# Kernel tuning notes

Hardware: AMD Instinct MI355X
Metric: run time of the kernel (lower is better)

Reference implementation:

```python
import jax, jax.numpy as jnp
from jax import lax
import numpy as np

B, C, H, W, OUTC, KS = 4, 64, 128, 128, 64, 3
N = KS * KS
PAD = 1
STRIDE = 1


def conv2d(x, w, b, stride, pad):
    out = lax.conv_general_dilated(x, w, (stride, stride), ((pad, pad), (pad, pad)),
                                   dimension_numbers=('NCHW', 'OIHW', 'NCHW'))
    if b is not None:
        out = out + b[None, :, None, None]
    return out


def setup_inputs() -> dict:
    key = jax.random.key(0)
    k = jax.random.split(key, 8)
    f = jnp.float32

    def w_init(kk, shape, fan_in, scale=1.0):
        return jax.random.normal(kk, shape, f) * (scale / np.sqrt(fan_in))

    return {
        'x': jax.random.normal(k[0], (B, C, H, W), f),
        'ref': jax.random.normal(k[1], (B, C, H, W), f),
        'w_cd': w_init(k[2], (C, 2 * C, 1, 1), 2 * C),
        'b_cd': jnp.zeros((C,), f),
        'w_p': w_init(k[3], (2 * N, C, 3, 3), C * 9, 0.1),  # small offsets, keeps sampling stable
        'b_p': jnp.zeros((2 * N,), f),
        'w_m': w_init(k[4], (N, C, 3, 3), C * 9),
        'b_m': jnp.zeros((N,), f),
        'w_c': w_init(k[5], (N * C, C, 3, 3), C * 9),
        'b_c': jnp.zeros((N * C,), f),
        'w_conv': w_init(k[6], (OUTC, C, KS, KS), C * KS * KS),
    }


def deform_forward(x, ref, w_cd, b_cd, w_p, b_p, w_m, b_m, w_c, b_c, w_conv):
    b, c, h, w = x.shape
    fused = conv2d(jnp.concatenate([x, ref], axis=1), w_cd, b_cd, 1, 0)
    offset = conv2d(fused, w_p, b_p, STRIDE, 1)             # [b, 2N, h, w]
    m = jax.nn.sigmoid(conv2d(fused, w_m, b_m, STRIDE, 1))  # [b, N, h, w]
    c_off = jnp.tanh(conv2d(fused, w_c, b_c, STRIDE, 1))    # [b, N*c, h, w]

    xp = jnp.pad(x, ((0, 0), (0, 0), (PAD, PAD), (PAD, PAD)))
    Hp, Wp = h + 2 * PAD, w + 2 * PAD

    # kernel-relative grid p_n (first N entries = rows, last N = cols)
    r = jnp.arange(-(KS - 1) // 2, (KS - 1) // 2 + 1)
    pnx, pny = jnp.meshgrid(r, r, indexing='ij')
    p_n = jnp.concatenate([pnx.ravel(), pny.ravel()]).reshape(1, 2 * N, 1, 1)
    # base grid p_0 starts at 1 because of the zero padding
    gx, gy = jnp.meshgrid(jnp.arange(1, h * STRIDE + 1, STRIDE),
                          jnp.arange(1, w * STRIDE + 1, STRIDE), indexing='ij')
    p_0 = jnp.concatenate([jnp.broadcast_to(gx[None, None], (1, N, h, w)),
                           jnp.broadcast_to(gy[None, None], (1, N, h, w))], axis=1)
    p = (p_0 + p_n).astype(offset.dtype) + offset           # [b, 2N, h, w]
    p = p.transpose(0, 2, 3, 1)                             # [b, h, w, 2N]

    q_lt = jnp.floor(lax.stop_gradient(p))
    q_rb = q_lt + 1

    def clampq(q):
        return jnp.concatenate([jnp.clip(q[..., :N], 0, Hp - 1),
                                jnp.clip(q[..., N:], 0, Wp - 1)], axis=-1).astype(jnp.int32)

    q_lt = clampq(q_lt)
    q_rb = clampq(q_rb)
    q_lb = jnp.concatenate([q_lt[..., :N], q_rb[..., N:]], axis=-1)
    q_rt = jnp.concatenate([q_rb[..., :N], q_lt[..., N:]], axis=-1)
    p = jnp.concatenate([jnp.clip(p[..., :N], 0, Hp - 1),
                         jnp.clip(p[..., N:], 0, Wp - 1)], axis=-1)

    def gweight(q, sx, sy):
        qx = q[..., :N].astype(p.dtype)
        qy = q[..., N:].astype(p.dtype)
        return (1 + sx * (qx - p[..., :N])) * (1 + sy * (qy - p[..., N:]))

    g_lt = gweight(q_lt, 1, 1)
    g_rb = gweight(q_rb, -1, -1)
    g_lb = gweight(q_lb, 1, -1)
    g_rt = gweight(q_rt, -1, 1)

    x_flat = xp.reshape(b, c, Hp * Wp)

    def get_x_q(q):
        idx = q[..., :N] * Wp + q[..., N:]                  # [b, h, w, N]
        xq = jnp.take_along_axis(x_flat, idx.reshape(b, 1, -1), axis=2)
        return xq.reshape(b, c, h, w, N)

    x_off = (g_lt[:, None] * get_x_q(q_lt) + g_rb[:, None] * get_x_q(q_rb)
             + g_lb[:, None] * get_x_q(q_lb) + g_rt[:, None] * get_x_q(q_rt))

    # color deformation: [b, N*c, h, w] -> [b, c, h, w, N]
    x_off = x_off + c_off.reshape(b, c, N, h, w).transpose(0, 1, 3, 4, 2)
    # modulation broadcast over channels
    x_off = x_off * m.transpose(0, 2, 3, 1)[:, None]

    # [b,c,h,w,N] -> [b,c,h*ks,w*ks] with N = (kernel_row, kernel_col)
    x_off = x_off.reshape(b, c, h, w, KS, KS).transpose(0, 1, 2, 4, 3, 5)
    x_off = x_off.reshape(b, c, h * KS, w * KS)
    return conv2d(x_off, w_conv, None, KS, 0)


def reference(x, ref, w_cd, b_cd, w_p, b_p, w_m, b_m, w_c, b_c, w_conv):
    return deform_forward(x, ref, w_cd, b_cd, w_p, b_p, w_m, b_m, w_c, b_c, w_conv)
```

## Files before the change

### kernel.cpp

```cpp
#include <hip/hip_runtime.h>
#include <hip/hip_fp16.h>


typedef __attribute__((ext_vector_type(8))) __bf16 bf16x8;
typedef __attribute__((ext_vector_type(16))) float f32x16;
#define MFMA32(a, b, c) __builtin_amdgcn_mfma_f32_32x32x16_bf16((a), (b), (c), 0, 0, 0)

#define WS_AC    0
#define WS_APM   368640
#define WS_ACONV 387072
#define WS_F2    436224

struct f2pair { float x, y; };

__device__ __forceinline__ unsigned short f2bf(float f) {
    unsigned u = __float_as_uint(f);
    return (unsigned short)((u + 0x7FFFu + ((u >> 16) & 1u)) >> 16);
}
__device__ __forceinline__ float fast_rcp(float x) {
#if __has_builtin(__builtin_amdgcn_rcpf)
    return __builtin_amdgcn_rcpf(x);
#else
    return 1.0f / x;
#endif
}
__device__ __forceinline__ float fast_tanh(float x) {
    float t = __expf(2.0f * x);
    return 1.0f - 2.0f * fast_rcp(t + 1.0f);
}
__device__ __forceinline__ float fast_sigmoid(float x) {
    return fast_rcp(1.0f + __expf(-x));
}

__device__ __forceinline__ uint4 stage_load64(const unsigned short* f2b, int h,
                                              int px0, int chunk, int tid) {
    int tap = chunk >> 1;
    int dh = tap / 3 - 1, dw = tap % 3 - 1;
    int hs = h + dh;
    int kg = tid >> 6, px = tid & 63;
    int cg = (chunk & 1) * 4 + kg;
    int wsrc = px0 + px + dw;
    uint4 pk = {0u, 0u, 0u, 0u};
    if (((unsigned)hs < 128u) && ((unsigned)wsrc < 128u))
        pk = *(const uint4*)(f2b + (((size_t)cg << 14) + (hs << 7) + wsrc) * 8);
    return pk;
}
__device__ __forceinline__ void stage_write64(char* Bst, uint4 pk, int tid) {
    int kg = tid >> 6, px = tid & 63;
    *(uint4*)(Bst + ((kg >> 1) * 2 + (px >> 5)) * 1024
                  + ((px & 31) + 32 * (kg & 1)) * 16) = pk;
}

__global__ __launch_bounds__(256, 4)
void k2_fused(const float* __restrict__ x, const float* __restrict__ ref,
              const float* __restrict__ b_cd, const float* __restrict__ w_c,
              const float* __restrict__ w_p, const float* __restrict__ w_m,
              const float* __restrict__ w_conv, const float* __restrict__ w_cd,
              unsigned short* __restrict__ ws) {
    __shared__ __align__(16) char B0[32768];
    __shared__ __align__(16) unsigned short WcdL[8192];
    const int tid = threadIdx.x, l = tid & 63, w = tid >> 6;
    const int b = blockIdx.y, p0 = blockIdx.x * 128;
    const int rl31 = l & 31, kh8 = (l >> 5) * 8;

    {
        int gtid = (blockIdx.y * 128 + blockIdx.x) * 256 + tid;
        #pragma unroll 1
        for (int i = gtid; i < 428032; i += 131072) {
            float val;
            if (i < WS_APM) {
                int t = i, jj = t & 7, lx = (t >> 3) & 63, r = t >> 9;
                int ks = r % 36, gmt = r / 36;
                int row = gmt * 32 + (lx & 31);
                int kp = ks * 16 + (lx >> 5) * 8 + jj, tap = kp >> 6, ci = kp & 63;
                val = (row < 576) ? w_c[row * 576 + ci * 9 + tap] : 0.0f;
            } else if (i < WS_ACONV) {
                int t = i - WS_APM, jj = t & 7, lx = (t >> 3) & 63, ks = t >> 9;
                int row = lx & 31;
                int kp = ks * 16 + (lx >> 5) * 8 + jj, tap = kp >> 6, ci = kp & 63;
                val = (row < 18) ? w_p[row * 576 + ci * 9 + tap]
                    : (row < 27) ? w_m[(row - 18) * 576 + ci * 9 + tap] : 0.0f;
            } else {
                int t = i - WS_ACONV, jj = t & 7, lx = (t >> 3) & 63, r = t >> 9;
                int gks = r % 40, ocT2 = r / 40;
                int oc = ocT2 * 32 + (lx & 31);
                int krow = gks * 16 + (lx >> 5) * 8 + jj;
                val = (krow < 576) ? w_conv[oc * 576 + krow] : 0.0f;
            }
            ws[i] = f2bf(val);
        }
    }
    #pragma unroll
    for (int i = tid; i < 8192; i += 256) WcdL[i] = f2bf(w_cd[i]);

    #pragma unroll
    for (int it = 0; it < 8; ++it) {
        int task = it * 256 + tid;
        int kg = task >> 7, px = task & 127;
        const float* src = (kg < 8) ? x : ref;
        int kbase = (kg & 7) * 8;
        unsigned short v[8];
        #pragma unroll
        for (int j = 0; j < 8; ++j)
            v[j] = f2bf(src[(((size_t)b * 64 + kbase + j) << 14) + p0 + px]);
        uint4 pk;
        pk.x = (unsigned)v[0] | ((unsigned)v[1] << 16);
        pk.y = (unsigned)v[2] | ((unsigned)v[3] << 16);
        pk.z = (unsigned)v[4] | ((unsigned)v[5] << 16);
        pk.w = (unsigned)v[6] | ((unsigned)v[7] << 16);
        *(uint4*)(B0 + ((kg >> 1) * 4 + (px >> 5)) * 1024
                      + ((px & 31) + 32 * (kg & 1)) * 16) = pk;
    }
    __syncthreads();

    f32x16 a0, a1;
    #pragma unroll
    for (int r = 0; r < 16; ++r) { a0[r] = 0.0f; a1[r] = 0.0f; }
    const unsigned short* A0 = WcdL + rl31 * 128 + kh8;
    #pragma unroll
    for (int s = 0; s < 8; ++s) {
        bf16x8 bf = *(bf16x8*)(B0 + ((s * 4 + w) * 64 + l) * 16);
        bf16x8 x0 = *(const bf16x8*)(A0 + s * 16);
        bf16x8 x1 = *(const bf16x8*)(A0 + 32 * 128 + s * 16);
        a0 = MFMA32(x0, bf, a0);
        a1 = MFMA32(x1, bf, a1);
    }
    unsigned short* f2 = ws + WS_F2 + ((size_t)b << 20);
    int px = p0 + w * 32 + rl31;
    int h4 = (l >> 5) * 4;
    #pragma unroll
    for (int t = 0; t < 2; ++t)
        #pragma unroll
        for (int q = 0; q < 4; ++q) {
            ushort4 st;
            float v0 = (t ? a1[q * 4 + 0] : a0[q * 4 + 0]) + b_cd[t * 32 + 8 * q + h4 + 0];
            float v1 = (t ? a1[q * 4 + 1] : a0[q * 4 + 1]) + b_cd[t * 32 + 8 * q + h4 + 1];
            float v2 = (t ? a1[q * 4 + 2] : a0[q * 4 + 2]) + b_cd[t * 32 + 8 * q + h4 + 2];
            float v3 = (t ? a1[q * 4 + 3] : a0[q * 4 + 3]) + b_cd[t * 32 + 8 * q + h4 + 3];
            st.x = f2bf(v0); st.y = f2bf(v1); st.z = f2bf(v2); st.w = f2bf(v3);
            *(ushort4*)(f2 + ((size_t)((t * 4 + q) << 14) + px) * 8 + h4) = st;
        }
}

__global__ __launch_bounds__(256, 4)
void k3_main(const float* __restrict__ x, const float* __restrict__ b_c,
             const float* __restrict__ b_p, const float* __restrict__ b_m,
             const unsigned short* __restrict__ wsbf, float* __restrict__ out) {
    __shared__ __align__(16) char lds[36096];
    char* Bst0 = lds;
    char* Bst1 = lds + 4096;
    char* Amod = lds + 8192;
    float* uL = (float*)(lds + 8192);
    char* tbl = lds + 24576;
    float* bcL = (float*)(lds + 33792);

    const int tid = threadIdx.x, l = tid & 63, w = tid >> 6;
    const int lh = l >> 5, l31 = l & 31;
    const int id = blockIdx.x;
    const int hbLin = (id & 7) * 128 + (id >> 3);
    const int half = hbLin & 1, b = (hbLin >> 1) & 3, h = hbLin >> 3;
    const int px0 = half * 64;
    const unsigned short* f2b = wsbf + WS_F2 + ((size_t)b << 20);
    const float* xb = x + (((size_t)b * 64) << 14);
    const int ocT = w >> 1, nT2 = w & 1;

    for (int i = tid; i < 576; i += 256) bcL[i] = b_c[i];

    f32x16 oa;

    auto epi = [&](f32x16& a, int j, int rowbase) {
        const int pxe = j * 32 + l31;
        if (rowbase < 576) {
            #pragma unroll
            for (int reg = 0; reg < 16; ++reg) {
                int rl = (reg & 3) + 8 * (reg >> 2) + 4 * lh;
                int row = rowbase + rl;
                int c = row / 9, n = row - c * 9;
                float uv = a[reg] + bcL[row];
                float t = fast_tanh(uv);
                uint4 rec = *(const uint4*)(tbl + (pxe * 9 + n) * 16);
                float w0 = __half2float(__ushort_as_half((unsigned short)(rec.x & 0xffffu)));
                float w1 = __half2float(__ushort_as_half((unsigned short)(rec.x >> 16)));
                float w2 = __half2float(__ushort_as_half((unsigned short)(rec.y & 0xffffu)));
                float w3 = __half2float(__ushort_as_half((unsigned short)(rec.y >> 16)));
                int i0 = (int)(rec.z & 0xffffu);
                int i1 = (int)(rec.z >> 16);
                float mval = __uint_as_float(rec.w);
                const float* xp = xb + ((size_t)c << 14);
                f2pair v0 = *(const f2pair*)(xp + i0);
                f2pair v1 = *(const f2pair*)(xp + i1);
                float samp = w0 * v0.x + w1 * v0.y + w2 * v1.x + w3 * v1.y;
                a[reg] = mval * (samp + t);
                if ((reg & 3) == 3) __builtin_amdgcn_sched_barrier(0);
            }
        } else {
            #pragma unroll
            for (int reg = 0; reg < 16; ++reg) a[reg] = 0.0f;
        }
    };
    auto scat = [&](const f32x16& a, int j) {
        #pragma unroll
        for (int reg = 0; reg < 16; ++reg) {
            int rl = (reg & 3) + 8 * (reg >> 2) + 4 * lh;
            int k = w * 32 + rl;
            *(unsigned short*)(Amod + ((k >> 4) * 2 + j) * 1024
                    + (l31 + 32 * ((k >> 3) & 1)) * 16 + (k & 7) * 2)
                = f2bf(a[reg]);
        }
    };

    {
        f32x16 acc0, acc1, pm;
        #pragma unroll
        for (int r = 0; r < 16; ++r) { acc0[r] = 0.0f; acc1[r] = 0.0f; pm[r] = 0.0f; }
        stage_write64(Bst0, stage_load64(f2b, h, px0, 0, tid), tid);
        __syncthreads();
        #pragma unroll 1
        for (int it = 0; it < 18; ++it) {
            char* cur = (it & 1) ? Bst1 : Bst0;
            char* nxt = (it & 1) ? Bst0 : Bst1;
            uint4 pk;
            if (it < 17) pk = stage_load64(f2b, h, px0, it + 1, tid);
            #pragma unroll
            for (int s = 0; s < 2; ++s) {
                const int ks = it * 2 + s;
                bf16x8 bf0 = *(bf16x8*)(cur + ((s * 2 + 0) * 64 + l) * 16);
                bf16x8 bf1 = *(bf16x8*)(cur + ((s * 2 + 1) * 64 + l) * 16);
                bf16x8 af = *(const bf16x8*)(wsbf + WS_AC
                                + (((w * 36 + ks) * 64 + l) << 3));
                acc0 = MFMA32(af, bf0, acc0);
                acc1 = MFMA32(af, bf1, acc1);
                if (w < 2) {
                    bf16x8 apm = *(const bf16x8*)(wsbf + WS_APM + ((ks * 64 + l) << 3));
                    pm = MFMA32(apm, w ? bf1 : bf0, pm);
                }
            }
            if (it < 17) stage_write64(nxt, pk, tid);
            __syncthreads();
        }
        if (w < 2) {
            int pxp = w * 32 + l31;
            #pragma unroll
            for (int reg = 0; reg < 16; ++reg) {
                int rl = (reg & 3) + 8 * (reg >> 2) + 4 * lh;
                uL[rl * 64 + pxp] = pm[reg];
            }
        }
        __syncthreads();

        #pragma unroll 1
        for (int i = tid; i < 576; i += 256) {
            int n = i >> 6, px = i & 63;
            float offr = uL[n * 64 + px] + b_p[n];
            float offc = uL[(9 + n) * 64 + px] + b_p[9 + n];
            float mraw = uL[(18 + n) * 64 + px] + b_m[n];
            int nr = n / 3, nc = n - nr * 3;
            float pr = (float)(h + nr) + offr;
            float pc = (float)(px0 + px + nc) + offc;
            float flr = floorf(pr), flc = floorf(pc);
            float prc = fminf(fmaxf(pr, 0.0f), 129.0f);
            float pcc = fminf(fmaxf(pc, 0.0f), 129.0f);
            float q0r = fminf(fmaxf(flr, 0.0f), 129.0f);
            float q1r = fminf(fmaxf(flr + 1.0f, 0.0f), 129.0f);
            int ir0 = (int)q0r, ir1 = (int)q1r;
            bool vr0 = (ir0 >= 1) && (ir0 <= 128), vr1 = (ir1 >= 1) && (ir1 <= 128);
            float wr0 = vr0 ? (1.0f + q0r - prc) : 0.0f;
            float wr1 = vr1 ? (1.0f - (q1r - prc)) : 0.0f;
            float q0c = fminf(fmaxf(flc, 0.0f), 129.0f);
            float q1c = fminf(fmaxf(flc + 1.0f, 0.0f), 129.0f);
            int ic0 = (int)q0c, ic1 = (int)q1c;
            bool vc0 = (ic0 >= 1) && (ic0 <= 128), vc1 = (ic1 >= 1) && (ic1 <= 128);
            float wc0 = vc0 ? (1.0f + q0c - pcc) : 0.0f;
            float wc1 = vc1 ? (1.0f - (q1c - pcc)) : 0.0f;
            int cx0 = ic0 - 1, cx1 = ic1 - 1;
            int base = min(max(cx0, 0), 126);
            float ws0 = ((base == cx0) && vc0 ? wc0 : 0.0f)
                      + ((base == cx1) && vc1 ? wc1 : 0.0f);
            float ws1 = ((base + 1 == cx0) && vc0 ? wc0 : 0.0f)
                      + ((base + 1 == cx1) && vc1 ? wc1 : 0.0f);
            int rx0 = min(max(ir0 - 1, 0), 127), rx1 = min(max(ir1 - 1, 0), 127);
            uint4 rec;
            rec.x = (unsigned)__half_as_ushort(__float2half(wr0 * ws0))
                  | ((unsigned)__half_as_ushort(__float2half(wr0 * ws1)) << 16);
            rec.y = (unsigned)__half_as_ushort(__float2half(wr1 * ws0))
                  | ((unsigned)__half_as_ushort(__float2half(wr1 * ws1)) << 16);
            rec.z = (unsigned)(unsigned short)(rx0 * 128 + base)
                  | ((unsigned)(unsigned short)(rx1 * 128 + base) << 16);
            rec.w = __float_as_uint(fast_sigmoid(mraw));
            *(uint4*)(tbl + (px * 9 + n) * 16) = rec;
        }
        __syncthreads();

        epi(acc0, 0, w * 32);
        epi(acc1, 1, w * 32);
        #pragma unroll
        for (int r = 0; r < 16; ++r) oa[r] = 0.0f;
        scat(acc0, 0);
        scat(acc1, 1);
        __syncthreads();
        #pragma unroll
        for (int ks8 = 0; ks8 < 8; ++ks8) {
            bf16x8 af = *(const bf16x8*)(wsbf + WS_ACONV
                            + (((ocT * 40 + ks8) * 64 + l) << 3));
            bf16x8 bf = *(bf16x8*)(Amod + (ks8 * 2 + nT2) * 1024 + l * 16);
            oa = MFMA32(af, bf, oa);
        }
    }

    #pragma unroll 1
    for (int p = 1; p < 5; ++p) {
        const int mt = p * 4 + w;
        f32x16 acc0, acc1;
        #pragma unroll
        for (int r = 0; r < 16; ++r) { acc0[r] = 0.0f; acc1[r] = 0.0f; }

        stage_write64(Bst0, stage_load64(f2b, h, px0, 0, tid), tid);
        __syncthreads();
        #pragma unroll 1
        for (int it = 0; it < 18; ++it) {
            char* cur = (it & 1) ? Bst1 : Bst0;
            char* nxt = (it & 1) ? Bst0 : Bst1;
            uint4 pk;
            if (it < 17) pk = stage_load64(f2b, h, px0, it + 1, tid);
            #pragma unroll
            for (int s = 0; s < 2; ++s) {
                const int ks = it * 2 + s;
                bf16x8 bf0 = *(bf16x8*)(cur + ((s * 2 + 0) * 64 + l) * 16);
                bf16x8 bf1 = *(bf16x8*)(cur + ((s * 2 + 1) * 64 + l) * 16);
                bf16x8 af = *(const bf16x8*)(wsbf + WS_AC
                                + (((mt * 36 + ks) * 64 + l) << 3));
                acc0 = MFMA32(af, bf0, acc0);
                acc1 = MFMA32(af, bf1, acc1);
            }
            if (it < 17) stage_write64(nxt, pk, tid);
            __syncthreads();
        }

        epi(acc0, 0, mt * 32);
        epi(acc1, 1, mt * 32);

        __syncthreads();
        scat(acc0, 0);
        scat(acc1, 1);
        __syncthreads();
        #pragma unroll
        for (int ks8 = 0; ks8 < 8; ++ks8) {
            bf16x8 af = *(const bf16x8*)(wsbf + WS_ACONV
                            + (((ocT * 40 + p * 8 + ks8) * 64 + l) << 3));
            bf16x8 bf = *(bf16x8*)(Amod + (ks8 * 2 + nT2) * 1024 + l * 16);
            oa = MFMA32(af, bf, oa);
        }
    }

    float* ob = out + (((size_t)b * 64) << 14) + (h << 7) + px0 + nT2 * 32 + l31;
    #pragma unroll
    for (int reg = 0; reg < 16; ++reg) {
        int rl = (reg & 3) + 8 * (reg >> 2) + 4 * lh;
        int oc = ocT * 32 + rl;
        ob[(size_t)oc << 14] = oa[reg];
    }
}

extern "C" void kernel_launch(void* const* d_in, const int* in_sizes, int n_in,
                              void* d_out, int out_size, void* d_ws, size_t ws_size,
                              hipStream_t stream) {
    const float* x      = (const float*)d_in[0];
    const float* ref    = (const float*)d_in[1];
    const float* w_cd   = (const float*)d_in[2];
    const float* b_cd   = (const float*)d_in[3];
    const float* w_p    = (const float*)d_in[4];
    const float* b_p    = (const float*)d_in[5];
    const float* w_m    = (const float*)d_in[6];
    const float* b_m    = (const float*)d_in[7];
    const float* w_c    = (const float*)d_in[8];
    const float* b_c    = (const float*)d_in[9];
    const float* w_conv = (const float*)d_in[10];
    float* out = (float*)d_out;
    unsigned short* wsbf = (unsigned short*)d_ws;

    hipLaunchKernelGGL(k2_fused, dim3(128, 4), dim3(256), 0, stream,
                       x, ref, b_cd, w_c, w_p, w_m, w_conv, w_cd, wsbf);
    hipLaunchKernelGGL(k3_main, dim3(1024), dim3(256), 0, stream,
                       x, b_c, b_p, b_m, wsbf, out);
}
```

Before: 233.6 us.

## Split offset/mask GEMM from first c-offset pass and vectorize input staging

```diff
diff --git a/kernel.cpp b/kernel.cpp
--- a/kernel.cpp
+++ b/kernel.cpp
@@ -30,6 +30,9 @@
 }
 __device__ __forceinline__ float fast_sigmoid(float x) {
     return fast_rcp(1.0f + __expf(-x));
+}
+__device__ __forceinline__ float comp4(const float4& v, int e) {
+    return (e == 0) ? v.x : (e == 1) ? v.y : (e == 2) ? v.z : v.w;
 }
 
 __device__ __forceinline__ uint4 stage_load64(const unsigned short* f2b, int h,
@@ -94,22 +97,30 @@
     for (int i = tid; i < 8192; i += 256) WcdL[i] = f2bf(w_cd[i]);
 
     #pragma unroll
-    for (int it = 0; it < 8; ++it) {
+    for (int it = 0; it < 2; ++it) {
         int task = it * 256 + tid;
-        int kg = task >> 7, px = task & 127;
+        int kg = task >> 5, pxg = task & 31;
         const float* src = (kg < 8) ? x : ref;
         int kbase = (kg & 7) * 8;
-        unsigned short v[8];
-        #pragma unroll
-        for (int j = 0; j < 8; ++j)
-            v[j] = f2bf(src[(((size_t)b * 64 + kbase + j) << 14) + p0 + px]);
-        uint4 pk;
-        pk.x = (unsigned)v[0] | ((unsigned)v[1] << 16);
-        pk.y = (unsigned)v[2] | ((unsigned)v[3] << 16);
-        pk.z = (unsigned)v[4] | ((unsigned)v[5] << 16);
-        pk.w = (unsigned)v[6] | ((unsigned)v[7] << 16);
-        *(uint4*)(B0 + ((kg >> 1) * 4 + (px >> 5)) * 1024
-                      + ((px & 31) + 32 * (kg & 1)) * 16) = pk;
+        const float* sp = src + (((size_t)b * 64 + kbase) << 14) + p0 + pxg * 4;
+        float4 v0 = *(const float4*)(sp);
+        float4 v1 = *(const float4*)(sp + (1 << 14));
+        float4 v2 = *(const float4*)(sp + (2 << 14));
+        float4 v3 = *(const float4*)(sp + (3 << 14));
+        float4 v4 = *(const float4*)(sp + (4 << 14));
+        float4 v5 = *(const float4*)(sp + (5 << 14));
+        float4 v6 = *(const float4*)(sp + (6 << 14));
+        float4 v7 = *(const float4*)(sp + (7 << 14));
+        char* bb = B0 + ((kg >> 1) * 4 + (pxg >> 3)) * 1024 + 32 * (kg & 1) * 16;
+        #pragma unroll
+        for (int e = 0; e < 4; ++e) {
+            uint4 pk;
+            pk.x = (unsigned)f2bf(comp4(v0, e)) | ((unsigned)f2bf(comp4(v1, e)) << 16);
+            pk.y = (unsigned)f2bf(comp4(v2, e)) | ((unsigned)f2bf(comp4(v3, e)) << 16);
+            pk.z = (unsigned)f2bf(comp4(v4, e)) | ((unsigned)f2bf(comp4(v5, e)) << 16);
+            pk.w = (unsigned)f2bf(comp4(v6, e)) | ((unsigned)f2bf(comp4(v7, e)) << 16);
+            *(uint4*)(bb + ((pxg & 7) * 4 + e) * 16) = pk;
+        }
     }
     __syncthreads();
 
@@ -166,53 +177,10 @@
 
     for (int i = tid; i < 576; i += 256) bcL[i] = b_c[i];
 
-    f32x16 oa;
-
-    auto epi = [&](f32x16& a, int j, int rowbase) {
-        const int pxe = j * 32 + l31;
-        if (rowbase < 576) {
-            #pragma unroll
-            for (int reg = 0; reg < 16; ++reg) {
-                int rl = (reg & 3) + 8 * (reg >> 2) + 4 * lh;
-                int row = rowbase + rl;
-                int c = row / 9, n = row - c * 9;
-                float uv = a[reg] + bcL[row];
-                float t = fast_tanh(uv);
-                uint4 rec = *(const uint4*)(tbl + (pxe * 9 + n) * 16);
-                float w0 = __half2float(__ushort_as_half((unsigned short)(rec.x & 0xffffu)));
-                float w1 = __half2float(__ushort_as_half((unsigned short)(rec.x >> 16)));
-                float w2 = __half2float(__ushort_as_half((unsigned short)(rec.y & 0xffffu)));
-                float w3 = __half2float(__ushort_as_half((unsigned short)(rec.y >> 16)));
-                int i0 = (int)(rec.z & 0xffffu);
-                int i1 = (int)(rec.z >> 16);
-                float mval = __uint_as_float(rec.w);
-                const float* xp = xb + ((size_t)c << 14);
-                f2pair v0 = *(const f2pair*)(xp + i0);
-                f2pair v1 = *(const f2pair*)(xp + i1);
-                float samp = w0 * v0.x + w1 * v0.y + w2 * v1.x + w3 * v1.y;
-                a[reg] = mval * (samp + t);
-                if ((reg & 3) == 3) __builtin_amdgcn_sched_barrier(0);
-            }
-        } else {
-            #pragma unroll
-            for (int reg = 0; reg < 16; ++reg) a[reg] = 0.0f;
-        }
-    };
-    auto scat = [&](const f32x16& a, int j) {
-        #pragma unroll
-        for (int reg = 0; reg < 16; ++reg) {
-            int rl = (reg & 3) + 8 * (reg >> 2) + 4 * lh;
-            int k = w * 32 + rl;
-            *(unsigned short*)(Amod + ((k >> 4) * 2 + j) * 1024
-                    + (l31 + 32 * ((k >> 3) & 1)) * 16 + (k & 7) * 2)
-                = f2bf(a[reg]);
-        }
-    };
-
     {
-        f32x16 acc0, acc1, pm;
-        #pragma unroll
-        for (int r = 0; r < 16; ++r) { acc0[r] = 0.0f; acc1[r] = 0.0f; pm[r] = 0.0f; }
+        f32x16 pm;
+        #pragma unroll
+        for (int r = 0; r < 16; ++r) pm[r] = 0.0f;
         stage_write64(Bst0, stage_load64(f2b, h, px0, 0, tid), tid);
         __syncthreads();
         #pragma unroll 1
@@ -221,18 +189,13 @@
             char* nxt = (it & 1) ? Bst0 : Bst1;
             uint4 pk;
             if (it < 17) pk = stage_load64(f2b, h, px0, it + 1, tid);
-            #pragma unroll
-            for (int s = 0; s < 2; ++s) {
-                const int ks = it * 2 + s;
-                bf16x8 bf0 = *(bf16x8*)(cur + ((s * 2 + 0) * 64 + l) * 16);
-                bf16x8 bf1 = *(bf16x8*)(cur + ((s * 2 + 1) * 64 + l) * 16);
-                bf16x8 af = *(const bf16x8*)(wsbf + WS_AC
-                                + (((w * 36 + ks) * 64 + l) << 3));
-                acc0 = MFMA32(af, bf0, acc0);
-                acc1 = MFMA32(af, bf1, acc1);
-                if (w < 2) {
+            if (w < 2) {
+                #pragma unroll
+                for (int s = 0; s < 2; ++s) {
+                    int ks = it * 2 + s;
+                    bf16x8 bf = *(bf16x8*)(cur + ((s * 2 + w) * 64 + l) * 16);
                     bf16x8 apm = *(const bf16x8*)(wsbf + WS_APM + ((ks * 64 + l) << 3));
-                    pm = MFMA32(apm, w ? bf1 : bf0, pm);
+                    pm = MFMA32(apm, bf, pm);
                 }
             }
             if (it < 17) stage_write64(nxt, pk, tid);
@@ -247,72 +210,63 @@
             }
         }
         __syncthreads();
-
-        #pragma unroll 1
-        for (int i = tid; i < 576; i += 256) {
-            int n = i >> 6, px = i & 63;
-            float offr = uL[n * 64 + px] + b_p[n];
-            float offc = uL[(9 + n) * 64 + px] + b_p[9 + n];
-            float mraw = uL[(18 + n) * 64 + px] + b_m[n];
-            int nr = n / 3, nc = n - nr * 3;
-            float pr = (float)(h + nr) + offr;
-            float pc = (float)(px0 + px + nc) + offc;
-            float flr = floorf(pr), flc = floorf(pc);
-            float prc = fminf(fmaxf(pr, 0.0f), 129.0f);
-            float pcc = fminf(fmaxf(pc, 0.0f), 129.0f);
-            float q0r = fminf(fmaxf(flr, 0.0f), 129.0f);
-            float q1r = fminf(fmaxf(flr + 1.0f, 0.0f), 129.0f);
-            int ir0 = (int)q0r, ir1 = (int)q1r;
-            bool vr0 = (ir0 >= 1) && (ir0 <= 128), vr1 = (ir1 >= 1) && (ir1 <= 128);
-            float wr0 = vr0 ? (1.0f + q0r - prc) : 0.0f;
-            float wr1 = vr1 ? (1.0f - (q1r - prc)) : 0.0f;
-            float q0c = fminf(fmaxf(flc, 0.0f), 129.0f);
-            float q1c = fminf(fmaxf(flc + 1.0f, 0.0f), 129.0f);
-            int ic0 = (int)q0c, ic1 = (int)q1c;
-            bool vc0 = (ic0 >= 1) && (ic0 <= 128), vc1 = (ic1 >= 1) && (ic1 <= 128);
-            float wc0 = vc0 ? (1.0f + q0c - pcc) : 0.0f;
-            float wc1 = vc1 ? (1.0f - (q1c - pcc)) : 0.0f;
-            int cx0 = ic0 - 1, cx1 = ic1 - 1;
-            int base = min(max(cx0, 0), 126);
-            float ws0 = ((base == cx0) && vc0 ? wc0 : 0.0f)
-                      + ((base == cx1) && vc1 ? wc1 : 0.0f);
-            float ws1 = ((base + 1 == cx0) && vc0 ? wc0 : 0.0f)
-                      + ((base + 1 == cx1) && vc1 ? wc1 : 0.0f);
-            int rx0 = min(max(ir0 - 1, 0), 127), rx1 = min(max(ir1 - 1, 0), 127);
-            uint4 rec;
-            rec.x = (unsigned)__half_as_ushort(__float2half(wr0 * ws0))
-                  | ((unsigned)__half_as_ushort(__float2half(wr0 * ws1)) << 16);
-            rec.y = (unsigned)__half_as_ushort(__float2half(wr1 * ws0))
-                  | ((unsigned)__half_as_ushort(__float2half(wr1 * ws1)) << 16);
-            rec.z = (unsigned)(unsigned short)(rx0 * 128 + base)
-                  | ((unsigned)(unsigned short)(rx1 * 128 + base) << 16);
-            rec.w = __float_as_uint(fast_sigmoid(mraw));
-            *(uint4*)(tbl + (px * 9 + n) * 16) = rec;
-        }
-        __syncthreads();
-
-        epi(acc0, 0, w * 32);
-        epi(acc1, 1, w * 32);
-        #pragma unroll
-        for (int r = 0; r < 16; ++r) oa[r] = 0.0f;
-        scat(acc0, 0);
-        scat(acc1, 1);
-        __syncthreads();
-        #pragma unroll
-        for (int ks8 = 0; ks8 < 8; ++ks8) {
-            bf16x8 af = *(const bf16x8*)(wsbf + WS_ACONV
-                            + (((ocT * 40 + ks8) * 64 + l) << 3));
-            bf16x8 bf = *(bf16x8*)(Amod + (ks8 * 2 + nT2) * 1024 + l * 16);
-            oa = MFMA32(af, bf, oa);
-        }
     }
 
     #pragma unroll 1
-    for (int p = 1; p < 5; ++p) {
+    for (int i = tid; i < 576; i += 256) {
+        int n = i >> 6, px = i & 63;
+        float offr = uL[n * 64 + px] + b_p[n];
+        float offc = uL[(9 + n) * 64 + px] + b_p[9 + n];
+        float mraw = uL[(18 + n) * 64 + px] + b_m[n];
+        int nr = n / 3, nc = n - nr * 3;
+        float pr = (float)(h + nr) + offr;
+        float pc = (float)(px0 + px + nc) + offc;
+        float flr = floorf(pr), flc = floorf(pc);
+        float prc = fminf(fmaxf(pr, 0.0f), 129.0f);
+        float pcc = fminf(fmaxf(pc, 0.0f), 129.0f);
+        float q0r = fminf(fmaxf(flr, 0.0f), 129.0f);
+        float q1r = fminf(fmaxf(flr + 1.0f, 0.0f), 129.0f);
+        int ir0 = (int)q0r, ir1 = (int)q1r;
+        bool vr0 = (ir0 >= 1) && (ir0 <= 128), vr1 = (ir1 >= 1) && (ir1 <= 128);
+        float wr0 = vr0 ? (1.0f + q0r - prc) : 0.0f;
+        float wr1 = vr1 ? (1.0f - (q1r - prc)) : 0.0f;
+        float q0c = fminf(fmaxf(flc, 0.0f), 129.0f);
+        float q1c = fminf(fmaxf(flc + 1.0f, 0.0f), 129.0f);
+        int ic0 = (int)q0c, ic1 = (int)q1c;
+        bool vc0 = (ic0 >= 1) && (ic0 <= 128), vc1 = (ic1 >= 1) && (ic1 <= 128);
+        float wc0 = vc0 ? (1.0f + q0c - pcc) : 0.0f;
+        float wc1 = vc1 ? (1.0f - (q1c - pcc)) : 0.0f;
+        int cx0 = ic0 - 1, cx1 = ic1 - 1;
+        int base = min(max(cx0, 0), 126);
+        float ws0 = ((base == cx0) && vc0 ? wc0 : 0.0f)
+                  + ((base == cx1) && vc1 ? wc1 : 0.0f);
+        float ws1 = ((base + 1 == cx0) && vc0 ? wc0 : 0.0f)
+                  + ((base + 1 == cx1) && vc1 ? wc1 : 0.0f);
+        int rx0 = min(max(ir0 - 1, 0), 127), rx1 = min(max(ir1 - 1, 0), 127);
+        uint4 rec;
+        rec.x = (unsigned)__half_as_ushort(__float2half(wr0 * ws0))
+              | ((unsigned)__half_as_ushort(__float2half(wr0 * ws1)) << 16);
+        rec.y = (unsigned)__half_as_ushort(__float2half(wr1 * ws0))
+              | ((unsigned)__half_as_ushort(__float2half(wr1 * ws1)) << 16);
+        rec.z = (unsigned)(unsigned short)(rx0 * 128 + base)
+              | ((unsigned)(unsigned short)(rx1 * 128 + base) << 16);
+        rec.w = __float_as_uint(fast_sigmoid(mraw));
+        *(uint4*)(tbl + (px * 9 + n) * 16) = rec;
+    }
+    __syncthreads();
+
+    f32x16 oa;
+    #pragma unroll
+    for (int r = 0; r < 16; ++r) oa[r] = 0.0f;
+
+    #pragma unroll 1
+    for (int p = 0; p < 5; ++p) {
         const int mt = p * 4 + w;
-        f32x16 acc0, acc1;
-        #pragma unroll
-        for (int r = 0; r < 16; ++r) { acc0[r] = 0.0f; acc1[r] = 0.0f; }
+        f32x16 acc[2];
+        #pragma unroll
+        for (int j = 0; j < 2; ++j)
+            #pragma unroll
+            for (int r = 0; r < 16; ++r) acc[j][r] = 0.0f;
 
         stage_write64(Bst0, stage_load64(f2b, h, px0, 0, tid), tid);
         __syncthreads();
@@ -329,19 +283,58 @@
                 bf16x8 bf1 = *(bf16x8*)(cur + ((s * 2 + 1) * 64 + l) * 16);
                 bf16x8 af = *(const bf16x8*)(wsbf + WS_AC
                                 + (((mt * 36 + ks) * 64 + l) << 3));
-                acc0 = MFMA32(af, bf0, acc0);
-                acc1 = MFMA32(af, bf1, acc1);
+                acc[0] = MFMA32(af, bf0, acc[0]);
+                acc[1] = MFMA32(af, bf1, acc[1]);
             }
             if (it < 17) stage_write64(nxt, pk, tid);
             __syncthreads();
         }
 
-        epi(acc0, 0, mt * 32);
-        epi(acc1, 1, mt * 32);
-
-        __syncthreads();
-        scat(acc0, 0);
-        scat(acc1, 1);
+        const int rowbase = mt * 32;
+        #pragma unroll
+        for (int j = 0; j < 2; ++j) {
+            const int pxe = j * 32 + l31;
+            if (rowbase < 576) {
+                #pragma unroll
+                for (int reg = 0; reg < 16; ++reg) {
+                    int rl = (reg & 3) + 8 * (reg >> 2) + 4 * lh;
+                    int row = rowbase + rl;
+                    int c = row / 9, n = row - c * 9;
+                    float uv = acc[j][reg] + bcL[row];
+                    float t = fast_tanh(uv);
+                    uint4 rec = *(const uint4*)(tbl + (pxe * 9 + n) * 16);
+                    float w0 = __half2float(__ushort_as_half((unsigned short)(rec.x & 0xffffu)));
+                    float w1 = __half2float(__ushort_as_half((unsigned short)(rec.x >> 16)));
+                    float w2 = __half2float(__ushort_as_half((unsigned short)(rec.y & 0xffffu)));
+                    float w3 = __half2float(__ushort_as_half((unsigned short)(rec.y >> 16)));
+                    int i0 = (int)(rec.z & 0xffffu);
+                    int i1 = (int)(rec.z >> 16);
+                    float mval = __uint_as_float(rec.w);
+                    const float* xp = xb + ((size_t)c << 14);
+                    f2pair v0 = *(const f2pair*)(xp + i0);
+                    f2pair v1 = *(const f2pair*)(xp + i1);
+                    float samp = w0 * v0.x + w1 * v0.y + w2 * v1.x + w3 * v1.y;
+                    acc[j][reg] = mval * (samp + t);
+                    if ((reg & 3) == 3) __builtin_amdgcn_sched_barrier(0);
+                }
+            } else {
+                #pragma unroll
+                for (int reg = 0; reg < 16; ++reg) acc[j][reg] = 0.0f;
+            }
+        }
+
+        __syncthreads();
+        #pragma unroll
+        for (int j = 0; j < 2; ++j) {
+            #pragma unroll
+            for (int reg = 0; reg < 16; ++reg) {
+                int rl = (reg & 3) + 8 * (reg >> 2) + 4 * lh;
+                int k = w * 32 + rl;
+                *(unsigned short*)(Amod + ((k >> 4) * 2 + j) * 1024
+                        + (l31 + 32 * ((k >> 3) & 1)) * 16 + (k & 7) * 2)
+                    = f2bf(acc[j][reg]);
+            }
+        }
         __syncthreads();
         #pragma unroll
         for (int ks8 = 0; ks8 < 8; ++ks8) {
```

Measured after the change: 234.3 us. About the same (+0.3%).
